# Performance work log

Hardware: AMD Instinct MI355X
Metric: run time of the kernel (lower is better)

Reference implementation:

```python
import jax, jax.numpy as jnp
import numpy as np

N_NODES = 50000
N_EDGES = 800000
HIDDEN = 128
OUT = 128


def setup_inputs() -> dict:
    key = jax.random.key(0)
    k1, k2, k3, k4, k5, k6 = jax.random.split(key, 6)
    h = jax.random.normal(k1, (N_NODES, HIDDEN), dtype=jnp.float32)
    src = jax.random.randint(k2, (N_EDGES,), 0, N_NODES, dtype=jnp.int64)
    dst = jax.random.randint(k3, (N_EDGES,), 0, N_NODES, dtype=jnp.int64)
    scale = 1.0 / np.sqrt(HIDDEN)
    W_edge = jax.random.normal(k4, (OUT, HIDDEN), dtype=jnp.float32) * scale
    W_self = jax.random.normal(k5, (OUT, HIDDEN), dtype=jnp.float32) * scale
    b_self = jax.random.normal(k6, (OUT,), dtype=jnp.float32) * scale
    return {"h": h, "src": src, "dst": dst, "W_edge": W_edge, "W_self": W_self, "b_self": b_self}


def reference(h, src, dst, W_edge, W_self, b_self):
    n = h.shape[0]
    # edge_transform(src_features): same linear on every edge -> transform nodes once, then gather
    msg_node = h @ W_edge.T                       # [N, OUT]
    msg = msg_node[src]                           # [E, OUT] gather
    sums = jax.ops.segment_sum(msg, dst, num_segments=n)  # [N, OUT] scatter-add
    deg = jax.ops.segment_sum(jnp.ones((dst.shape[0],), dtype=h.dtype), dst, num_segments=n)
    h1 = sums / jnp.maximum(deg, 1.0)[:, None]    # mean; zero in-degree -> 0 (DGL semantics)
    out = jax.nn.relu(h @ W_self.T + b_self + h1)
    return out
```

## Files before the change

kernel.cpp:

```cpp
#include <hip/hip_runtime.h>

#define N_HID 128
#define CAP   32
#define OVF_CAP 8192
#define NSLICE 8
#define PBLK   256

typedef short bf16x8 __attribute__((ext_vector_type(8)));
typedef float f32x4  __attribute__((ext_vector_type(4)));

static __device__ __forceinline__ unsigned short f2bf(float f)
{
    unsigned int u = __float_as_uint(f);
    u = (u + 0x7fffu + ((u >> 16) & 1u)) >> 16;
    return (unsigned short)u;
}
static __device__ __forceinline__ unsigned int pack2(float a, float b)
{
    return (unsigned int)f2bf(a) | ((unsigned int)f2bf(b) << 16);
}
static __device__ __forceinline__ float bf2f(unsigned int bits16)
{
    return __uint_as_float(bits16 << 16);
}
static __device__ __forceinline__ int slice_of(int d, float sln)
{
    int sl = (int)((float)d * sln);
    return sl > NSLICE - 1 ? NSLICE - 1 : sl;
}

__global__ __launch_bounds__(256) void count_fragw_cast(
    const int* __restrict__ dst, int* __restrict__ blockCnt,
    int* __restrict__ cnt, int* __restrict__ ovfn, int E, int n, float sln,
    const float* __restrict__ We, const float* __restrict__ Ws,
    unsigned short* __restrict__ Be, unsigned short* __restrict__ Bs,
    const float* __restrict__ h, unsigned short* __restrict__ hbf, int total)
{
    int t = threadIdx.x, b = blockIdx.x;

    if (b >= PBLK + 16) {
        int idx = (b - PBLK - 16) * 2048 + t * 8;
        if (idx + 8 <= total) {
            float4 v0 = *(const float4*)&h[idx];
            float4 v1 = *(const float4*)&h[idx + 4];
            uint4 pk;
            pk.x = pack2(v0.x, v0.y);
            pk.y = pack2(v0.z, v0.w);
            pk.z = pack2(v1.x, v1.y);
            pk.w = pack2(v1.z, v1.w);
            *(uint4*)&hbf[idx] = pk;
        }
        return;
    }

    if (b >= PBLK) {
        int bb = b - PBLK;
        const float* srcw = (bb < 8) ? We : Ws;
        unsigned short* dstF = (bb < 8) ? Be : Bs;
        int rt = bb & 7;
        int kc = t >> 6, l = t & 63, m = l & 15, q = l >> 4;
        const float* p = &srcw[(size_t)(rt * 16 + m) * N_HID + kc * 32 + q * 8];
        float4 v0 = *(const float4*)p;
        float4 v1 = *(const float4*)(p + 4);
        uint4 pk;
        pk.x = pack2(v0.x, v0.y);
        pk.y = pack2(v0.z, v0.w);
        pk.z = pack2(v1.x, v1.y);
        pk.w = pack2(v1.z, v1.w);
        *(uint4*)&dstF[(size_t)rt * 2048 + kc * 512 + l * 8] = pk;
        return;
    }

    for (int i = b * 256 + t; i < n; i += PBLK * 256) cnt[i] = 0;
    if (b == 0 && t == 0) *ovfn = 0;

    int c[NSLICE];
#pragma unroll
    for (int s = 0; s < NSLICE; ++s) c[s] = 0;

    for (int e = b * 256 + t; e < E; e += PBLK * 256) {
        int sl = slice_of(dst[e], sln);
#pragma unroll
        for (int s = 0; s < NSLICE; ++s) c[s] += (sl == s);
    }

    __shared__ int red[NSLICE * 4];
    int lane = t & 63, wid = t >> 6;
#pragma unroll
    for (int s = 0; s < NSLICE; ++s) {
        int v = c[s];
#pragma unroll
        for (int off = 32; off; off >>= 1) v += __shfl_down(v, off);
        if (lane == 0) red[s * 4 + wid] = v;
    }
    __syncthreads();
    if (t < NSLICE)
        blockCnt[t * PBLK + b] = red[t*4+0] + red[t*4+1] + red[t*4+2] + red[t*4+3];
}

__global__ __launch_bounds__(256) void part_scan(
    const int* __restrict__ blockCnt, int* __restrict__ blockBase,
    int* __restrict__ sbase, int E)
{
    __shared__ int wsm[4];
    int t = threadIdx.x, lane = t & 63, wid = t >> 6;
    int v[8]; int s = 0;
#pragma unroll
    for (int i = 0; i < 8; ++i) { v[i] = blockCnt[t * 8 + i]; s += v[i]; }
    int val = s;
#pragma unroll
    for (int off = 1; off < 64; off <<= 1) {
        int y = __shfl_up(val, off);
        if (lane >= off) val += y;
    }
    if (lane == 63) wsm[wid] = val;
    __syncthreads();
    if (t == 0) { int a = 0; for (int w = 0; w < 4; ++w) { int tmp = wsm[w]; wsm[w] = a; a += tmp; } }
    __syncthreads();
    int excl = wsm[wid] + val - s;
#pragma unroll
    for (int i = 0; i < 8; ++i) { int tv = v[i]; blockBase[t * 8 + i] = excl; excl += tv; }
    __syncthreads();
    if (t < NSLICE) sbase[t] = blockBase[t * PBLK];
    if (t == 0)     sbase[NSLICE] = E;
}

__global__ __launch_bounds__(256) void part_scatter(
    const int* __restrict__ src, const int* __restrict__ dst,
    const int* __restrict__ blockBase, unsigned int* __restrict__ part,
    int E, int n, float sln)
{
    __shared__ int cur[NSLICE];
    int t = threadIdx.x, b = blockIdx.x;
    if (t < NSLICE) cur[t] = blockBase[t * PBLK + b];
    __syncthreads();
    for (int e = b * 256 + t; e < E; e += PBLK * 256) {
        int d = dst[e], s = src[e];
        int sl  = slice_of(d, sln);
        int pos = atomicAdd(&cur[sl], 1);
        part[pos] = ((unsigned int)d << 16) | (unsigned int)s;
    }
}

__global__ __launch_bounds__(256) void bucket_scatter2(
    const unsigned int* __restrict__ part,
    const int* __restrict__ sbase,
    int* __restrict__ cnt,
    unsigned short* __restrict__ bucket,
    int* __restrict__ ovfn,
    long long* __restrict__ ovf)
{
    const int slice = blockIdx.x & 7;
    const int g     = blockIdx.x >> 3;
    const int nG    = (int)(gridDim.x >> 3);
    const int lo    = sbase[slice];
    const int hi    = sbase[slice + 1];
    const int m     = hi - lo;

    const int chunk = (m + nG - 1) / nG;
    const int e0 = lo + g * chunk;
    int e1 = e0 + chunk; if (e1 > hi) e1 = hi;

    for (int e = e0 + (int)threadIdx.x; e < e1; e += 256) {
        unsigned int pk = part[e];
        int d = (int)(pk >> 16);
        int s = (int)(pk & 0xffffu);
        int c = atomicAdd(&cnt[d], 1);
        if (c < CAP) {
            bucket[(size_t)d * CAP + c] = (unsigned short)s;
        } else {
            int o = atomicAdd(ovfn, 1);
            if (o < OVF_CAP) ovf[o] = ((long long)d << 32) | (unsigned int)s;
        }
    }
}

__global__ __launch_bounds__(256) void gather_gemm(
    const int* __restrict__ cnt,
    const unsigned short* __restrict__ bucket,
    const int* __restrict__ ovfn,
    const long long* __restrict__ ovf,
    const unsigned short* __restrict__ hbf,
    const unsigned short* __restrict__ Be,
    const unsigned short* __restrict__ Bsf,
    const float* __restrict__ bias,
    float* __restrict__ out,
    int n, int nrt)
{
    __shared__ __align__(16) unsigned int wl[16 * 68];

    const int t    = threadIdx.x;
    const int wid  = t >> 6;
    const int lane = t & 63;
    const int slice = blockIdx.x & 7;
    const int g     = blockIdx.x >> 3;
    const int tLo = (int)(((long long)slice * nrt) >> 3);
    const int tHi = (int)(((long long)(slice + 1) * nrt) >> 3);
    const int tile = tLo + g;
    if (tile >= tHi) return;

    const unsigned int* h32 = (const unsigned int*)hbf;

#pragma unroll
    for (int k = 0; k < 4; ++k) {
        int mm = wid * 4 + k;
        int node = tile * 16 + mm;
        float ax = 0.f, ay = 0.f;
        if (node < n) {
            int deg = cnt[node];
            int m = deg < CAP ? deg : CAP;
            const unsigned short* bk = &bucket[(size_t)node * CAP];

            int i = 0;
            for (; i + 8 <= m; i += 8) {
                uint4 b4 = *(const uint4*)&bk[i];
                unsigned int r0 = b4.x & 0xffffu, r1 = b4.x >> 16;
                unsigned int r2 = b4.y & 0xffffu, r3 = b4.y >> 16;
                unsigned int r4 = b4.z & 0xffffu, r5 = b4.z >> 16;
                unsigned int r6 = b4.w & 0xffffu, r7 = b4.w >> 16;
                unsigned int v0 = h32[(size_t)r0 * 64 + lane];
                unsigned int v1 = h32[(size_t)r1 * 64 + lane];
                unsigned int v2 = h32[(size_t)r2 * 64 + lane];
                unsigned int v3 = h32[(size_t)r3 * 64 + lane];
                unsigned int v4 = h32[(size_t)r4 * 64 + lane];
                unsigned int v5 = h32[(size_t)r5 * 64 + lane];
                unsigned int v6 = h32[(size_t)r6 * 64 + lane];
                unsigned int v7 = h32[(size_t)r7 * 64 + lane];
                ax += bf2f(v0 & 0xffffu) + bf2f(v1 & 0xffffu)
                    + bf2f(v2 & 0xffffu) + bf2f(v3 & 0xffffu)
                    + bf2f(v4 & 0xffffu) + bf2f(v5 & 0xffffu)
                    + bf2f(v6 & 0xffffu) + bf2f(v7 & 0xffffu);
                ay += bf2f(v0 >> 16) + bf2f(v1 >> 16)
                    + bf2f(v2 >> 16) + bf2f(v3 >> 16)
                    + bf2f(v4 >> 16) + bf2f(v5 >> 16)
                    + bf2f(v6 >> 16) + bf2f(v7 >> 16);
            }
            for (; i + 4 <= m; i += 4) {
                ushort4 ss = *(const ushort4*)&bk[i];
                unsigned int v0 = h32[(size_t)ss.x * 64 + lane];
                unsigned int v1 = h32[(size_t)ss.y * 64 + lane];
                unsigned int v2 = h32[(size_t)ss.z * 64 + lane];
                unsigned int v3 = h32[(size_t)ss.w * 64 + lane];
                ax += bf2f(v0 & 0xffffu) + bf2f(v1 & 0xffffu)
                    + bf2f(v2 & 0xffffu) + bf2f(v3 & 0xffffu);
                ay += bf2f(v0 >> 16) + bf2f(v1 >> 16)
                    + bf2f(v2 >> 16) + bf2f(v3 >> 16);
            }
            for (; i < m; ++i) {
                unsigned int v = h32[(size_t)bk[i] * 64 + lane];
                ax += bf2f(v & 0xffffu);
                ay += bf2f(v >> 16);
            }

            if (deg > CAP) {
                int no = *ovfn; if (no > OVF_CAP) no = OVF_CAP;
                for (int o = 0; o < no; ++o) {
                    long long pk = ovf[o];
                    if ((int)(pk >> 32) == node) {
                        unsigned int v = h32[(size_t)(unsigned int)pk * 64 + lane];
                        ax += bf2f(v & 0xffffu);
                        ay += bf2f(v >> 16);
                    }
                }
            }
            float sc = deg > 0 ? 1.0f / (float)deg : 0.f;
            ax *= sc; ay *= sc;
        }
        wl[mm * 68 + lane] = pack2(ax, ay);
    }
    __syncthreads();

    const int rr = lane & 15, q = lane >> 4;
    const int row0 = tile * 16;

    bf16x8 ah[4], ag[4];
#pragma unroll
    for (int kc = 0; kc < 4; ++kc) {
        int gr = row0 + rr; if (gr > n - 1) gr = n - 1;
        ah[kc] = *(const bf16x8*)&hbf[(size_t)gr * N_HID + kc * 32 + q * 8];
        ag[kc] = *(const bf16x8*)&wl[rr * 68 + kc * 16 + q * 4];
    }

    const int colb = lane & 15;
    const int rq   = (lane >> 4) * 4;

#pragma unroll
    for (int cti = 0; cti < 2; ++cti) {
        int ct = wid * 2 + cti;
        const bf16x8* BpS = (const bf16x8*)(Bsf + (size_t)ct * 2048);
        const bf16x8* BpE = (const bf16x8*)(Be  + (size_t)ct * 2048);
        f32x4 acc = {0.f, 0.f, 0.f, 0.f};
        acc = __builtin_amdgcn_mfma_f32_16x16x32_bf16(ah[0], BpS[lane],       acc, 0, 0, 0);
        acc = __builtin_amdgcn_mfma_f32_16x16x32_bf16(ah[1], BpS[64 + lane],  acc, 0, 0, 0);
        acc = __builtin_amdgcn_mfma_f32_16x16x32_bf16(ah[2], BpS[128 + lane], acc, 0, 0, 0);
        acc = __builtin_amdgcn_mfma_f32_16x16x32_bf16(ah[3], BpS[192 + lane], acc, 0, 0, 0);
        acc = __builtin_amdgcn_mfma_f32_16x16x32_bf16(ag[0], BpE[lane],       acc, 0, 0, 0);
        acc = __builtin_amdgcn_mfma_f32_16x16x32_bf16(ag[1], BpE[64 + lane],  acc, 0, 0, 0);
        acc = __builtin_amdgcn_mfma_f32_16x16x32_bf16(ag[2], BpE[128 + lane], acc, 0, 0, 0);
        acc = __builtin_amdgcn_mfma_f32_16x16x32_bf16(ag[3], BpE[192 + lane], acc, 0, 0, 0);

        int col = ct * 16 + colb;
        float bv = bias[col];
#pragma unroll
        for (int r = 0; r < 4; ++r) {
            int row = row0 + rq + r;
            if (row < n) out[(size_t)row * N_HID + col] = fmaxf(acc[r] + bv, 0.f);
        }
    }
}

extern "C" void kernel_launch(void* const* d_in, const int* in_sizes, int n_in,
                              void* d_out, int out_size, void* d_ws, size_t ws_size,
                              hipStream_t stream)
{
    const float* h   = (const float*)d_in[0];
    const int*   src = (const int*)d_in[1];
    const int*   dst = (const int*)d_in[2];
    const float* We  = (const float*)d_in[3];
    const float* Ws  = (const float*)d_in[4];
    const float* bs  = (const float*)d_in[5];
    float*       out = (float*)d_out;

    const int n   = in_sizes[0] / N_HID;
    const int E   = in_sizes[1];
    const int nrt = (n + 15) / 16;
    const float sln = (float)NSLICE / (float)n;
    const int total = n * N_HID;

    unsigned short* hbf  = (unsigned short*)d_ws;
    unsigned short* bucket = hbf + (size_t)n * N_HID;
    unsigned short* Be  = bucket + (size_t)n * CAP;
    unsigned short* Bs  = Be + 8 * 2048;
    int*  cnt  = (int*)(Bs + 8 * 2048);
    int*  ovfn = cnt + n;
    long long* ovf = (long long*)(ovfn + 8);
    int*  blockCnt  = (int*)(ovf + OVF_CAP);
    int*  blockBase = blockCnt + PBLK * NSLICE;
    int*  sbase     = blockBase + PBLK * NSLICE;
    unsigned int* part = (unsigned int*)(sbase + 16);

    const int castBlocks = (total + 2047) / 2048;

    const int maxTilesPerSlice = (nrt + NSLICE - 1) / NSLICE;
    const int ggGrid = NSLICE * maxTilesPerSlice;

    count_fragw_cast<<<PBLK + 16 + castBlocks, 256, 0, stream>>>(
        dst, blockCnt, cnt, ovfn, E, n, sln, We, Ws, Be, Bs, h, hbf, total);
    part_scan<<<1, 256, 0, stream>>>(blockCnt, blockBase, sbase, E);
    part_scatter<<<PBLK, 256, 0, stream>>>(src, dst, blockBase, part, E, n, sln);
    bucket_scatter2<<<1024, 256, 0, stream>>>(part, sbase, cnt, bucket, ovfn, ovf);
    gather_gemm<<<ggGrid, 256, 0, stream>>>(cnt, bucket, ovfn, ovf,
                                            hbf, Be, Bs, bs, out, n, nrt);
}
```

Measured before the change: 183.4 us.

## Gather neighbor rows with 16-byte loads across quarter-waves and shuffle reduction

Restructures the per-node neighbor aggregation so each quarter-wave of 16 lanes fetches a whole 256-byte bf16 row with uint4 loads. One wave therefore gathers four neighbors per load instruction instead of one, and the partial sums are combined with xor shuffles. Degree counts and bucket indices are loaded once per wave up front and broadcast with shuffles, replacing per-node scalar loads. The aim is fewer, wider gather loads and more memory parallelism. The cost is extra shuffle reductions, more accumulator registers, and redundant masked loads on the tail of each 16-edge chunk.

Result: faster. 174.4 us (-4.9%).

```diff
diff --git a/kernel.cpp b/kernel.cpp
--- a/kernel.cpp
+++ b/kernel.cpp
@@ -192,6 +192,8 @@
     const int t    = threadIdx.x;
     const int wid  = t >> 6;
     const int lane = t & 63;
+    const int q    = lane >> 4;
+    const int s    = lane & 15;
     const int slice = blockIdx.x & 7;
     const int g     = blockIdx.x >> 3;
     const int tLo = (int)(((long long)slice * nrt) >> 3);
@@ -199,86 +201,91 @@
     const int tile = tLo + g;
     if (tile >= tHi) return;
 
+    const uint4* h4 = (const uint4*)hbf;
     const unsigned int* h32 = (const unsigned int*)hbf;
 
+    const int nodeBase = tile * 16 + wid * 4;
+    int cntv = cnt[tile * 16 + s];
+    unsigned int bkv = ((const unsigned int*)bucket)[(size_t)nodeBase * 16 + lane];
+
 #pragma unroll
     for (int k = 0; k < 4; ++k) {
-        int mm = wid * 4 + k;
-        int node = tile * 16 + mm;
-        float ax = 0.f, ay = 0.f;
+        const int mm   = wid * 4 + k;
+        const int node = tile * 16 + mm;
+        float a0=0.f,a1=0.f,a2=0.f,a3=0.f,a4=0.f,a5=0.f,a6=0.f,a7=0.f;
+        int deg = 0;
         if (node < n) {
-            int deg = cnt[node];
+            deg = __shfl(cntv, mm);
             int m = deg < CAP ? deg : CAP;
-            const unsigned short* bk = &bucket[(size_t)node * CAP];
-
-            int i = 0;
-            for (; i + 8 <= m; i += 8) {
-                uint4 b4 = *(const uint4*)&bk[i];
-                unsigned int r0 = b4.x & 0xffffu, r1 = b4.x >> 16;
-                unsigned int r2 = b4.y & 0xffffu, r3 = b4.y >> 16;
-                unsigned int r4 = b4.z & 0xffffu, r5 = b4.z >> 16;
-                unsigned int r6 = b4.w & 0xffffu, r7 = b4.w >> 16;
-                unsigned int v0 = h32[(size_t)r0 * 64 + lane];
-                unsigned int v1 = h32[(size_t)r1 * 64 + lane];
-                unsigned int v2 = h32[(size_t)r2 * 64 + lane];
-                unsigned int v3 = h32[(size_t)r3 * 64 + lane];
-                unsigned int v4 = h32[(size_t)r4 * 64 + lane];
-                unsigned int v5 = h32[(size_t)r5 * 64 + lane];
-                unsigned int v6 = h32[(size_t)r6 * 64 + lane];
-                unsigned int v7 = h32[(size_t)r7 * 64 + lane];
-                ax += bf2f(v0 & 0xffffu) + bf2f(v1 & 0xffffu)
-                    + bf2f(v2 & 0xffffu) + bf2f(v3 & 0xffffu)
-                    + bf2f(v4 & 0xffffu) + bf2f(v5 & 0xffffu)
-                    + bf2f(v6 & 0xffffu) + bf2f(v7 & 0xffffu);
-                ay += bf2f(v0 >> 16) + bf2f(v1 >> 16)
-                    + bf2f(v2 >> 16) + bf2f(v3 >> 16)
-                    + bf2f(v4 >> 16) + bf2f(v5 >> 16)
-                    + bf2f(v6 >> 16) + bf2f(v7 >> 16);
-            }
-            for (; i + 4 <= m; i += 4) {
-                ushort4 ss = *(const ushort4*)&bk[i];
-                unsigned int v0 = h32[(size_t)ss.x * 64 + lane];
-                unsigned int v1 = h32[(size_t)ss.y * 64 + lane];
-                unsigned int v2 = h32[(size_t)ss.z * 64 + lane];
-                unsigned int v3 = h32[(size_t)ss.w * 64 + lane];
-                ax += bf2f(v0 & 0xffffu) + bf2f(v1 & 0xffffu)
-                    + bf2f(v2 & 0xffffu) + bf2f(v3 & 0xffffu);
-                ay += bf2f(v0 >> 16) + bf2f(v1 >> 16)
-                    + bf2f(v2 >> 16) + bf2f(v3 >> 16);
-            }
-            for (; i < m; ++i) {
-                unsigned int v = h32[(size_t)bk[i] * 64 + lane];
-                ax += bf2f(v & 0xffffu);
-                ay += bf2f(v >> 16);
+            const int kb = k * 16;
+
+            for (int base = 0; base < m; base += 16) {
+                uint4 vr[4]; unsigned int vm[4];
+#pragma unroll
+                for (int i = 0; i < 4; ++i) {
+                    int idx = base + i * 4 + q;
+                    int c   = idx < m ? idx : m - 1;
+                    unsigned int wsel = (unsigned int)__shfl((int)bkv, kb + (c >> 1));
+                    unsigned int r    = (c & 1) ? (wsel >> 16) : (wsel & 0xffffu);
+                    vr[i] = h4[(size_t)r * 16 + s];
+                    vm[i] = (idx < m) ? 0xffffffffu : 0u;
+                }
+#pragma unroll
+                for (int i = 0; i < 4; ++i) {
+                    unsigned int x;
+                    x = vr[i].x & vm[i]; a0 += bf2f(x & 0xffffu); a1 += bf2f(x >> 16);
+                    x = vr[i].y & vm[i]; a2 += bf2f(x & 0xffffu); a3 += bf2f(x >> 16);
+                    x = vr[i].z & vm[i]; a4 += bf2f(x & 0xffffu); a5 += bf2f(x >> 16);
+                    x = vr[i].w & vm[i]; a6 += bf2f(x & 0xffffu); a7 += bf2f(x >> 16);
+                }
             }
 
             if (deg > CAP) {
                 int no = *ovfn; if (no > OVF_CAP) no = OVF_CAP;
+                unsigned int qm = (q == 0) ? 0xffffffffu : 0u;
                 for (int o = 0; o < no; ++o) {
                     long long pk = ovf[o];
                     if ((int)(pk >> 32) == node) {
-                        unsigned int v = h32[(size_t)(unsigned int)pk * 64 + lane];
-                        ax += bf2f(v & 0xffffu);
-                        ay += bf2f(v >> 16);
+                        uint4 v = h4[(size_t)(unsigned int)pk * 16 + s];
+                        unsigned int x;
+                        x = v.x & qm; a0 += bf2f(x & 0xffffu); a1 += bf2f(x >> 16);
+                        x = v.y & qm; a2 += bf2f(x & 0xffffu); a3 += bf2f(x >> 16);
+                        x = v.z & qm; a4 += bf2f(x & 0xffffu); a5 += bf2f(x >> 16);
+                        x = v.w & qm; a6 += bf2f(x & 0xffffu); a7 += bf2f(x >> 16);
                     }
                 }
             }
-            float sc = deg > 0 ? 1.0f / (float)deg : 0.f;
-            ax *= sc; ay *= sc;
-        }
-        wl[mm * 68 + lane] = pack2(ax, ay);
-    }
-    __syncthreads();
-
-    const int rr = lane & 15, q = lane >> 4;
+        }
+
+#pragma unroll
+        for (int off = 16; off <= 32; off <<= 1) {
+            a0 += __shfl_xor(a0, off); a1 += __shfl_xor(a1, off);
+            a2 += __shfl_xor(a2, off); a3 += __shfl_xor(a3, off);
+            a4 += __shfl_xor(a4, off); a5 += __shfl_xor(a5, off);
+            a6 += __shfl_xor(a6, off); a7 += __shfl_xor(a7, off);
+        }
+
+        float sc = deg > 0 ? 1.0f / (float)deg : 0.f;
+        if (q == 0) {
+            uint4 pk;
+            pk.x = pack2(a0 * sc, a1 * sc);
+            pk.y = pack2(a2 * sc, a3 * sc);
+            pk.z = pack2(a4 * sc, a5 * sc);
+            pk.w = pack2(a6 * sc, a7 * sc);
+            *(uint4*)&wl[mm * 68 + 4 * s] = pk;
+        }
+    }
+    __syncthreads();
+
+    const int rr = lane & 15, qq = lane >> 4;
     const int row0 = tile * 16;
 
     bf16x8 ah[4], ag[4];
 #pragma unroll
     for (int kc = 0; kc < 4; ++kc) {
         int gr = row0 + rr; if (gr > n - 1) gr = n - 1;
-        ah[kc] = *(const bf16x8*)&hbf[(size_t)gr * N_HID + kc * 32 + q * 8];
-        ag[kc] = *(const bf16x8*)&wl[rr * 68 + kc * 16 + q * 4];
+        ah[kc] = *(const bf16x8*)&hbf[(size_t)gr * N_HID + kc * 32 + qq * 8];
+        ag[kc] = *(const bf16x8*)&wl[rr * 68 + kc * 16 + qq * 4];
     }
 
     const int colb = lane & 15;
```
